# Performance work log

Hardware: AMD Instinct MI355X
Metric: run time of the kernel (lower is better)

## Reference

```python
import jax, jax.numpy as jnp
import numpy as np

NUM_HEADS = 12   # top-k = num_heads experts selected per token
SWITCHLOSS = 0.1
ZLOSS = 0.001


def setup_inputs() -> dict:
    key = jax.random.key(0)
    ks = jax.random.split(key, 8)
    B, N, C, E, D = 2, 2048, 768, 24, 64
    w = lambda k, shape: (jax.random.normal(k, shape, jnp.float32) * 0.02)
    return {
        "x": jax.random.normal(ks[0], (B, N, C), jnp.float32),
        "w_gate": w(ks[1], (C, E)),
        "W_in": w(ks[2], (E, C, D)),    # per-expert q projection
        "b_in": jnp.zeros((E, D), jnp.float32),
        "W_out": w(ks[3], (E, D, C)),   # per-expert output projection
        "b_out": jnp.zeros((E, C), jnp.float32),
        "W_kv": w(ks[4], (C, 2 * D)),   # shared single-head K/V
        "b_kv": jnp.zeros((2 * D,), jnp.float32),
    }


def reference(x, w_gate, W_in, b_in, W_out, b_out, W_kv, b_kv):
    B, N, C = x.shape
    E, _, D = W_in.shape
    H = NUM_HEADS
    scale = D ** -0.5

    xf = x.reshape(-1, C)                         # [T, C], T = B*N
    # --- top-k gating (k = num_heads) ---
    logits = xf @ w_gate                          # [T, E]
    probs = jax.nn.softmax(logits, axis=-1)
    top_p, idx = jax.lax.top_k(probs, H)          # [T, H]
    gates = top_p / (top_p.sum(-1, keepdims=True) + 1e-6)
    oh = jax.nn.one_hot(idx, E, dtype=x.dtype)    # [T, H, E]
    comb = oh * gates[..., None]                  # gated dispatch/combine weights

    # --- aux losses (switchloss + zloss; cvloss coeff = 0) ---
    dense_gates = comb.sum(1)                     # [T, E]
    freqs = (dense_gates > 0).astype(x.dtype).sum(0)
    p_sum = probs.sum(0)
    switch = E * jnp.sum((p_sum / p_sum.sum()) * (freqs / freqs.sum()))
    z = jnp.mean(jax.nn.logsumexp(logits, axis=1) ** 2)
    aux_loss = SWITCHLOSS * switch + ZLOSS * z

    # --- MoE map: per-token q via selected experts (no gate multiply) ---
    q_all = jnp.einsum('tc,ecd->ted', xf, W_in) + b_in     # [T, E, D]
    q = jnp.take_along_axis(q_all, idx[..., None], axis=1)  # [T, H, D]
    q = q.reshape(B, N, H, D)

    # --- shared-KV attention (multi-query style) ---
    kv = x @ W_kv + b_kv
    k, v = jnp.split(kv, 2, axis=-1)              # [B, N, D] each
    attn = jnp.einsum('bihd,bjd->bhij', q, k) * scale
    attn = jax.nn.softmax(attn, axis=-1)
    o = jnp.einsum('bhij,bjd->bihd', attn, v).reshape(-1, H, D)  # [T, H, D]

    # --- MoE reduce: gated combine through per-expert output projections ---
    xe = jnp.einsum('the,thd->ted', comb, o)      # [T, E, D] gated dispatch
    out = jnp.einsum('ted,edc->tc', xe, W_out) + jnp.einsum('the,ec->tc', comb, b_out)
    return out.reshape(B, N, C), aux_loss
```

## Files before the change

kernel.cpp:

```cpp
#include <hip/hip_runtime.h>
#include <hip/hip_bf16.h>

#define T_  4096
#define Bb  2
#define Nn  2048
#define Cc  768
#define Ee  24
#define Dd  64
#define Hh  12
#define KR  1600
#define KS  16
#define KC  48
#define NB2 1024
#define SCL 0.18033688f

typedef __attribute__((ext_vector_type(8))) short bf16x8;
typedef __attribute__((ext_vector_type(4))) short bf16x4;
typedef __attribute__((ext_vector_type(4))) float f32x4;
typedef __attribute__((ext_vector_type(8))) unsigned short u16x8;

__device__ __forceinline__ unsigned short f2bf(float f) {
  union { float f; unsigned int i; } u; u.f = f;
  unsigned int r = u.i + 0x7FFFu + ((u.i >> 16) & 1u);
  return (unsigned short)(r >> 16);
}

__device__ __forceinline__ void gload16(const void* g, void* l) {
  __builtin_amdgcn_global_load_lds(
      (const __attribute__((address_space(1))) void*)g,
      (__attribute__((address_space(3))) void*)l, 16, 0, 0);
}

#define XPAD 52
__global__ __launch_bounds__(256) void prep_kernel(
    const float* __restrict__ W_in, const float* __restrict__ W_out,
    const float* __restrict__ b_out, const float* __restrict__ W_kv,
    unsigned short* __restrict__ BqT, unsigned short* __restrict__ BrT,
    unsigned short* __restrict__ BkvT,
    const float* __restrict__ x, const float* __restrict__ wg,
    float* __restrict__ partial, unsigned short* __restrict__ xb)
{
  __shared__ __align__(16) float smem[64 * 129];
  const int bid = blockIdx.x, tid = threadIdx.x;

  if (bid < 900) {
    float* ls = smem;
    if (bid < 288) {
      const int e = bid / 12, c0 = (bid % 12) * 64;
      #pragma unroll
      for (int i = 0; i < 16; ++i) {
        int L = tid + i * 256, c = L >> 6, d = L & 63;
        ls[c * 65 + d] = W_in[(size_t)e * Cc * Dd + (size_t)(c0 + c) * Dd + d];
      }
      __syncthreads();
      #pragma unroll
      for (int i = 0; i < 16; ++i) {
        int L = tid + i * 256, d = L >> 6, c = L & 63;
        BqT[(size_t)(e * Dd + d) * Cc + c0 + c] = f2bf(ls[c * 65 + d]);
      }
    } else if (bid < 888) {
      const int i2 = bid - 288;
      const int k0 = (i2 / 12) * 32, n0 = (i2 % 12) * 64;
      #pragma unroll
      for (int i = 0; i < 8; ++i) {
        int L = tid + i * 256, k = L >> 6, n = L & 63;
        int kk = k0 + k;
        float v = (kk < 1536) ? W_out[(size_t)kk * Cc + n0 + n]
                : (kk < 1560) ? b_out[(size_t)(kk - 1536) * Cc + n0 + n] : 0.f;
        ls[k * 65 + n] = v;
      }
      __syncthreads();
      #pragma unroll
      for (int i = 0; i < 8; ++i) {
        int L = tid + i * 256, n = L >> 5, k = L & 31;
        BrT[(size_t)(n0 + n) * KR + k0 + k] = f2bf(ls[k * 65 + n]);
      }
    } else {
      const int c0 = (bid - 888) * 64;
      #pragma unroll
      for (int i = 0; i < 32; ++i) {
        int L = tid + i * 256, c = L >> 7, j = L & 127;
        ls[c * 129 + j] = W_kv[(size_t)(c0 + c) * 128 + j];
      }
      __syncthreads();
      #pragma unroll
      for (int i = 0; i < 32; ++i) {
        int L = tid + i * 256, j = L >> 6, c = L & 63;
        BkvT[(size_t)j * Cc + c0 + c] = f2bf(ls[c * 129 + j]);
      }
    }
  } else {
    float* xs  = smem;
    float* wsT = smem + 128 * XPAD;
    const int g = bid - 900;
    const int t0 = (g & 31) * 128;
    const int s = g >> 5, k0 = s * KC;

    #pragma unroll
    for (int i = 0; i < 6; ++i) {
      int f = tid + i * 256;
      int token = f / 12, j = f % 12;
      size_t gofs = (size_t)(t0 + token) * Cc + k0 + j * 4;
      float4 v = *(const float4*)&x[gofs];
      *(float4*)&xs[token * XPAD + j * 4] = v;
      ushort4 o;
      o.x = f2bf(v.x); o.y = f2bf(v.y); o.z = f2bf(v.z); o.w = f2bf(v.w);
      *(ushort4*)&xb[gofs] = o;
    }
    for (int i = tid; i < Ee * KC; i += 256)
      wsT[(i % Ee) * KC + i / Ee] = wg[k0 * Ee + i];
    __syncthreads();

    const int token = tid >> 1, half = tid & 1;
    float xr[KC];
    #pragma unroll
    for (int kg = 0; kg < KC / 4; ++kg)
      *(float4*)&xr[kg * 4] = *(const float4*)&xs[token * XPAD + kg * 4];

    float acc[12];
    #pragma unroll
    for (int e = 0; e < 12; ++e) acc[e] = 0.f;
    #pragma unroll
    for (int e = 0; e < 12; ++e) {
      const int eg = half * 12 + e;
      #pragma unroll
      for (int kg = 0; kg < KC / 4; ++kg) {
        float4 wv = *(const float4*)&wsT[eg * KC + kg * 4];
        acc[e] += xr[kg * 4 + 0] * wv.x + xr[kg * 4 + 1] * wv.y
                + xr[kg * 4 + 2] * wv.z + xr[kg * 4 + 3] * wv.w;
      }
    }

    float* dst = partial + ((size_t)(t0 + token) * KS + s) * Ee + half * 12;
    #pragma unroll
    for (int eg2 = 0; eg2 < 3; ++eg2)
      *(float4*)&dst[eg2 * 4] = *(float4*)&acc[eg2 * 4];
  }
}

template<int MODE>
__global__ __launch_bounds__(256) void gemm_bt_kernel(
    const unsigned short* __restrict__ A, const unsigned short* __restrict__ BT,
    const float* __restrict__ bias, const float* __restrict__ bias2,
    void* __restrict__ Cout, void* __restrict__ Cout2, void* __restrict__ Cout3,
    int K, int ldc)
{
  constexpr int BM = 64, BN = 64, MI = 2, NI = 2;
  __shared__ __align__(16) unsigned short As[2][BM * 64];
  __shared__ __align__(16) unsigned short Bs[2][BN * 64];
  const int tid = threadIdx.x, w = tid >> 6, lane = tid & 63;
  const int quad = lane >> 4, nl = lane & 15;
  const int m0 = blockIdx.x * BM, n0 = blockIdx.y * BN;
  const int mw = (w & 1) * 32, nw = (w >> 1) * 32;

  f32x4 acc[MI][NI];
  #pragma unroll
  for (int i = 0; i < MI; ++i)
    #pragma unroll
    for (int j = 0; j < NI; ++j) acc[i][j] = (f32x4){0.f, 0.f, 0.f, 0.f};

  const int sr  = lane >> 3;
  const int cbd = (lane & 7) ^ sr;
  const int xl  = nl & 7;
  const int ca0 = (quad ^ xl) * 8;
  const int ca1 = ((quad + 4) ^ xl) * 8;

  const unsigned short* abase = A + (size_t)(m0 + w * 16 + sr) * K + cbd * 8;
  const unsigned short* bbase = BT + (size_t)(n0 + w * 16 + sr) * K + cbd * 8;

  auto STAGE = [&](int bi, int k0) {
    #pragma unroll
    for (int i = 0; i < 2; ++i) {
      gload16(abase + (size_t)(i * 8) * K + k0, &As[bi][(w * 16 + i * 8) * 64]);
      gload16(bbase + (size_t)(i * 8) * K + k0, &Bs[bi][(w * 16 + i * 8) * 64]);
    }
  };

  const int nt = K / 64;
  STAGE(0, 0);
  __syncthreads();
  for (int t = 0; t < nt; ++t) {
    const int cur = t & 1;
    if (t + 1 < nt) STAGE(cur ^ 1, (t + 1) * 64);

    bf16x8 af0[MI], af1[MI], bf0[NI], bf1[NI];
    #pragma unroll
    for (int mi = 0; mi < MI; ++mi) {
      const unsigned short* ar = &As[cur][(mw + mi * 16 + nl) * 64];
      af0[mi] = *(const bf16x8*)(ar + ca0);
      af1[mi] = *(const bf16x8*)(ar + ca1);
    }
    #pragma unroll
    for (int ni = 0; ni < NI; ++ni) {
      const unsigned short* br = &Bs[cur][(nw + ni * 16 + nl) * 64];
      bf0[ni] = *(const bf16x8*)(br + ca0);
      bf1[ni] = *(const bf16x8*)(br + ca1);
    }
    #pragma unroll
    for (int mi = 0; mi < MI; ++mi)
      #pragma unroll
      for (int ni = 0; ni < NI; ++ni) {
        acc[mi][ni] = __builtin_amdgcn_mfma_f32_16x16x32_bf16(
            af0[mi], bf0[ni], acc[mi][ni], 0, 0, 0);
        acc[mi][ni] = __builtin_amdgcn_mfma_f32_16x16x32_bf16(
            af1[mi], bf1[ni], acc[mi][ni], 0, 0, 0);
      }

    __syncthreads();
  }

  #pragma unroll
  for (int mi = 0; mi < MI; ++mi) {
    int rowb = m0 + mw + mi * 16 + quad * 4;
    int bb = rowb >> 11, nn = rowb & (Nn - 1);
    #pragma unroll
    for (int ni = 0; ni < NI; ++ni) {
      int col = n0 + nw + ni * 16 + nl;
      if (MODE == 0) {
        #pragma unroll
        for (int reg = 0; reg < 4; ++reg)
          ((float*)Cout)[(size_t)(rowb + reg) * ldc + col] = acc[mi][ni][reg];
      } else {
        if (col < 1536) {
          float bv = bias[col];
          #pragma unroll
          for (int reg = 0; reg < 4; ++reg)
            ((unsigned short*)Cout)[(size_t)(rowb + reg) * 1536 + col] =
                f2bf((acc[mi][ni][reg] + bv) * SCL);
        } else {
          int c2 = col - 1536;
          float bv = bias2[c2];
          if (c2 < Dd) {
            #pragma unroll
            for (int reg = 0; reg < 4; ++reg)
              ((unsigned short*)Cout2)[((size_t)bb * Nn + nn + reg) * Dd + c2] =
                  f2bf(acc[mi][ni][reg] + bv);
          } else {
            int p6 = nn & 63;
            int np = (nn & ~63) | (p6 & 0x23)
                   | (((p6 >> 4) & 1) << 2) | (((p6 >> 2) & 3) << 3);
            ushort4 v;
            v.x = f2bf(acc[mi][ni][0] + bv);
            v.y = f2bf(acc[mi][ni][1] + bv);
            v.z = f2bf(acc[mi][ni][2] + bv);
            v.w = f2bf(acc[mi][ni][3] + bv);
            *(ushort4*)((unsigned short*)Cout3 +
                        ((size_t)bb * Dd + (c2 - Dd)) * Nn + np) = v;
          }
        }
      }
    }
  }
}

__global__ __launch_bounds__(256) void gate2_kernel(
    const float* __restrict__ partial,
    int* __restrict__ idx, float* __restrict__ gate, float* __restrict__ bstats,
    unsigned short* __restrict__ xeg)
{
  __shared__ float xls[4][KS * Ee];
  __shared__ float sacc[49];
  __shared__ unsigned short dens[4][64];
  const int tid = threadIdx.x;
  const int w = tid >> 6, lane = tid & 63;
  const int t = blockIdx.x * 4 + w;

  if (tid < 49) sacc[tid] = 0.f;
  dens[w][lane] = 0;

  const float* p = partial + (size_t)t * (KS * Ee);
  #pragma unroll
  for (int i = 0; i < 6; ++i) xls[w][lane + i * 64] = p[lane + i * 64];

  {
    u16x8 z = (u16x8){0, 0, 0, 0, 0, 0, 0, 0};
    unsigned short* xrow = xeg + (size_t)t * KR;
    #pragma unroll
    for (int i = 0; i < 3; ++i)
      *(u16x8*)&xrow[(lane + i * 64) * 8] = z;
  }

  float logit = -1e30f;
  if (lane < Ee) {
    float acc = 0.f;
    #pragma unroll
    for (int s = 0; s < KS; ++s) acc += xls[w][s * Ee + lane];
    logit = acc;
  }
  float m = logit;
  for (int o = 32; o; o >>= 1) m = fmaxf(m, __shfl_xor(m, o));
  float pr = (lane < Ee) ? expf(logit - m) : 0.f;
  float s = pr;
  for (int o = 32; o; o >>= 1) s += __shfl_xor(s, o);
  float prob = pr / s;
  float lse = m + logf(s);

  bool sel = false;
  float my_p = 0.f; int my_e = -1;
  for (int h = 0; h < Hh; ++h) {
    float v = (lane < Ee && !sel) ? prob : -1.f;
    int ix = lane;
    for (int o = 32; o; o >>= 1) {
      float ov = __shfl_xor(v, o); int oi = __shfl_xor(ix, o);
      if (ov > v || (ov == v && oi < ix)) { v = ov; ix = oi; }
    }
    if (lane == ix) sel = true;
    if (lane == h) { my_p = v; my_e = ix; }
  }
  float gsum = (lane < Hh) ? my_p : 0.f;
  for (int o = 32; o; o >>= 1) gsum += __shfl_xor(gsum, o);
  float gval = my_p / (gsum + 1e-6f);
  if (lane < Hh) {
    idx[t * Hh + lane] = my_e;
    gate[t * Hh + lane] = gval;
  }

  __syncthreads();
  if (lane < Ee) atomicAdd(&sacc[lane], prob);
  if (lane < Hh) {
    atomicAdd(&sacc[24 + my_e], 1.0f);
    dens[w][my_e] = f2bf(gval);
  }
  if (lane == 0) atomicAdd(&sacc[48], lse * lse);
  __syncthreads();
  if (tid < 49) bstats[(size_t)tid * NB2 + blockIdx.x] = sacc[tid];

  xeg[(size_t)t * KR + 1536 + lane] = dens[w][lane];
}

__global__ __launch_bounds__(256, 3) void attn_kernel(
    const unsigned short* __restrict__ qallb, const int* __restrict__ idx,
    const float* __restrict__ gate,
    const unsigned short* __restrict__ kbuf, const unsigned short* __restrict__ vtbuf,
    unsigned short* __restrict__ xeg)
{
  __shared__ __align__(16) unsigned short ksl[3][64 * 64];
  __shared__ __align__(16) unsigned short vtl[3][64 * 64];

  const int tid = threadIdx.x;
  const int w = tid >> 6, lane = tid & 63;
  const int quad = lane >> 4, nl = lane & 15;
  const int bh = blockIdx.y;
  const int b = bh / Hh, h = bh - b * Hh;
  const int qw = blockIdx.x * 64 + w * 16;

  const int tq = b * Nn + qw + nl;
  const int eq = idx[tq * Hh + h];
  const unsigned short* qrow = qallb + (size_t)tq * (Ee * Dd) + eq * Dd + quad * 8;
  const bf16x8 qB0 = *(const bf16x8*)(qrow);
  const bf16x8 qB1 = *(const bf16x8*)(qrow + 32);

  f32x4 acc[4];
  #pragma unroll
  for (int dg = 0; dg < 4; ++dg) acc[dg] = (f32x4){0.f, 0.f, 0.f, 0.f};
  float l = 0.f;

  const int sr  = lane >> 3;
  const int cbd = (lane & 7) ^ sr;
  const int xl  = nl & 7;
  const int ca0 = (quad ^ xl) * 8;
  const int ca1 = ((quad + 4) ^ xl) * 8;

  const unsigned short* kgbase =
      kbuf + ((size_t)b * Nn + w * 16 + sr) * Dd + cbd * 8;
  const unsigned short* vgbase =
      vtbuf + ((size_t)b * Dd + w * 16 + sr) * Nn + cbd * 8;

  auto STAGE = [&](int bi, int t) {
    const int j0 = t * 64;
    #pragma unroll
    for (int i = 0; i < 2; ++i) {
      gload16(kgbase + (size_t)(j0 + i * 8) * Dd, &ksl[bi][(w * 16 + i * 8) * 64]);
      gload16(vgbase + (size_t)(i * 8) * Nn + j0, &vtl[bi][(w * 16 + i * 8) * 64]);
    }
  };

  auto COMPUTE = [&](const unsigned short* ks_, const unsigned short* vt_) {
    __builtin_amdgcn_s_setprio(1);
    bf16x4 pf[4];
    #pragma unroll
    for (int kg = 0; kg < 4; ++kg) {
      const unsigned short* kr = ks_ + (kg * 16 + nl) * 64;
      bf16x8 a0 = *(const bf16x8*)(kr + ca0);
      bf16x8 a1 = *(const bf16x8*)(kr + ca1);
      f32x4 c = {0.f, 0.f, 0.f, 0.f};
      c = __builtin_amdgcn_mfma_f32_16x16x32_bf16(a0, qB0, c, 0, 0, 0);
      c = __builtin_amdgcn_mfma_f32_16x16x32_bf16(a1, qB1, c, 0, 0, 0);
      float p0 = __builtin_amdgcn_exp2f(c[0]);
      float p1 = __builtin_amdgcn_exp2f(c[1]);
      float p2 = __builtin_amdgcn_exp2f(c[2]);
      float p3 = __builtin_amdgcn_exp2f(c[3]);
      l += (p0 + p1) + (p2 + p3);
      union { __hip_bfloat162 h2[2]; bf16x4 v; } pk;
      pk.h2[0] = __float22bfloat162_rn(float2{p0, p1});
      pk.h2[1] = __float22bfloat162_rn(float2{p2, p3});
      pf[kg] = pk.v;
    }
    bf16x8 pb0 = __builtin_shufflevector(pf[0], pf[1], 0, 1, 2, 3, 4, 5, 6, 7);
    bf16x8 pb1 = __builtin_shufflevector(pf[2], pf[3], 0, 1, 2, 3, 4, 5, 6, 7);
    #pragma unroll
    for (int dg = 0; dg < 4; ++dg) {
      const unsigned short* vrow = vt_ + (dg * 16 + nl) * 64;
      bf16x8 v0 = *(const bf16x8*)(vrow + ca0);
      bf16x8 v1 = *(const bf16x8*)(vrow + ca1);
      acc[dg] = __builtin_amdgcn_mfma_f32_16x16x32_bf16(v0, pb0, acc[dg], 0, 0, 0);
      acc[dg] = __builtin_amdgcn_mfma_f32_16x16x32_bf16(v1, pb1, acc[dg], 0, 0, 0);
    }
    __builtin_amdgcn_s_setprio(0);
  };

  STAGE(0, 0);
  STAGE(1, 1);
  #pragma unroll 1
  for (int t = 0; t < 30; t += 3) {
    STAGE(2, t + 2);
    asm volatile("s_waitcnt vmcnt(8)" ::: "memory");
    __builtin_amdgcn_s_barrier();
    __builtin_amdgcn_sched_barrier(0);
    COMPUTE(ksl[0], vtl[0]);
    __builtin_amdgcn_sched_barrier(0);
    asm volatile("" ::: "memory");
    __builtin_amdgcn_s_barrier();

    STAGE(0, t + 3);
    asm volatile("s_waitcnt vmcnt(8)" ::: "memory");
    __builtin_amdgcn_s_barrier();
    __builtin_amdgcn_sched_barrier(0);
    COMPUTE(ksl[1], vtl[1]);
    __builtin_amdgcn_sched_barrier(0);
    asm volatile("" ::: "memory");
    __builtin_amdgcn_s_barrier();

    STAGE(1, t + 4);
    asm volatile("s_waitcnt vmcnt(8)" ::: "memory");
    __builtin_amdgcn_s_barrier();
    __builtin_amdgcn_sched_barrier(0);
    COMPUTE(ksl[2], vtl[2]);
    __builtin_amdgcn_sched_barrier(0);
    asm volatile("" ::: "memory");
    __builtin_amdgcn_s_barrier();
  }
  asm volatile("s_waitcnt vmcnt(4)" ::: "memory");
  __builtin_amdgcn_s_barrier();
  __builtin_amdgcn_sched_barrier(0);
  COMPUTE(ksl[0], vtl[0]);
  __builtin_amdgcn_sched_barrier(0);
  asm volatile("s_waitcnt vmcnt(0)" ::: "memory");
  __builtin_amdgcn_s_barrier();
  __builtin_amdgcn_sched_barrier(0);
  COMPUTE(ksl[1], vtl[1]);

  float lg = l;
  lg += __shfl_xor(lg, 16);
  lg += __shfl_xor(lg, 32);
  const float scale = gate[tq * Hh + h] / lg;
  unsigned short* xrow = xeg + (size_t)tq * KR + eq * Dd + quad * 4;
  #pragma unroll
  for (int dg = 0; dg < 4; ++dg) {
    ushort4 v;
    v.x = f2bf(acc[dg][0] * scale);
    v.y = f2bf(acc[dg][1] * scale);
    v.z = f2bf(acc[dg][2] * scale);
    v.w = f2bf(acc[dg][3] * scale);
    *(ushort4*)(xrow + dg * 16) = v;
  }
}

__global__ __launch_bounds__(256) void aux1_kernel(
    const float* __restrict__ bstats, float* __restrict__ stats2)
{
  __shared__ float r[4];
  const int j = blockIdx.x, tid = threadIdx.x;
  float4 v = *(const float4*)&bstats[(size_t)j * NB2 + tid * 4];
  float s = (v.x + v.y) + (v.z + v.w);
  for (int o = 32; o; o >>= 1) s += __shfl_xor(s, o);
  if ((tid & 63) == 0) r[tid >> 6] = s;
  __syncthreads();
  if (tid == 0) stats2[j] = (r[0] + r[1]) + (r[2] + r[3]);
}

__global__ void aux2_kernel(const float* __restrict__ stats2,
                            float* __restrict__ out, int out_size)
{
  const int lane = threadIdx.x;
  float a = (lane < Ee) ? stats2[lane] : 0.f;
  float b = (lane < Ee) ? stats2[24 + lane] : 0.f;
  float pt = a, ft = b, sw = a * b;
  for (int o = 32; o; o >>= 1) {
    pt += __shfl_xor(pt, o); ft += __shfl_xor(ft, o); sw += __shfl_xor(sw, o);
  }
  if (lane == 0) {
    float sswitch = (float)Ee * sw / (pt * ft);
    float z = stats2[48] * (1.0f / (float)T_);
    out[out_size - 1] = 0.1f * sswitch + 0.001f * z;
  }
}

extern "C" void kernel_launch(void* const* d_in, const int* in_sizes, int n_in,
                              void* d_out, int out_size, void* d_ws, size_t ws_size,
                              hipStream_t stream)
{
  const float* x     = (const float*)d_in[0];
  const float* wg    = (const float*)d_in[1];
  const float* W_in  = (const float*)d_in[2];
  const float* b_in  = (const float*)d_in[3];
  const float* W_out = (const float*)d_in[4];
  const float* b_out = (const float*)d_in[5];
  const float* W_kv  = (const float*)d_in[6];
  const float* b_kv  = (const float*)d_in[7];
  float* out = (float*)d_out;

  char* ws = (char*)d_ws;
  size_t off = 0;
  auto carve = [&](size_t bytes) -> void* {
    void* p = ws + off;
    off = (off + bytes + 255) & ~(size_t)255;
    return p;
  };
  int*            idx    = (int*)           carve((size_t)T_ * Hh * 4);
  float*          gate   = (float*)         carve((size_t)T_ * Hh * 4);
  float*          bstats = (float*)         carve((size_t)49 * NB2 * 4);
  float*          stats2 = (float*)         carve(256);
  float*          lgate  = (float*)         carve((size_t)T_ * KS * Ee * 4);
  unsigned short* xb     = (unsigned short*)carve((size_t)T_ * Cc * 2);
  unsigned short* BqkvT  = (unsigned short*)carve((size_t)(Ee * Dd + 128) * Cc * 2);
  unsigned short* BkvT   = BqkvT + (size_t)Ee * Dd * Cc;
  unsigned short* BrT    = (unsigned short*)carve((size_t)Cc * KR * 2);
  unsigned short* kbuf   = (unsigned short*)carve((size_t)T_ * Dd * 2);
  unsigned short* vtbuf  = (unsigned short*)carve((size_t)T_ * Dd * 2);
  unsigned short* qallb  = (unsigned short*)carve((size_t)T_ * Ee * Dd * 2);
  unsigned short* xeg    = (unsigned short*)carve((size_t)T_ * KR * 2);

  prep_kernel<<<1412, 256, 0, stream>>>(
      W_in, W_out, b_out, W_kv, BqkvT, BrT, BkvT, x, wg, lgate, xb);

  gate2_kernel<<<NB2, 256, 0, stream>>>(lgate, idx, gate, bstats, xeg);

  gemm_bt_kernel<1><<<dim3(T_ / 64, 26), 256, 0, stream>>>(
      xb, BqkvT, b_in, b_kv, qallb, kbuf, vtbuf, Cc, 1536);

  attn_kernel<<<dim3(Nn / 64, Bb * Hh), 256, 0, stream>>>(
      qallb, idx, gate, kbuf, vtbuf, xeg);

  gemm_bt_kernel<0><<<dim3(T_ / 64, Cc / 64), 256, 0, stream>>>(
      xeg, BrT, nullptr, nullptr, out, nullptr, nullptr, KR, Cc);

  aux1_kernel<<<49, 256, 0, stream>>>(bstats, stats2);
  aux2_kernel<<<1, 64, 0, stream>>>(stats2, out, out_size);
}
```

Measured before the change: 179.6 us.

## Merge independent gating and GEMM launches into combined heterogeneous grids

The gate-selection kernel and the QKV projection GEMM are folded into one launch, with blocks dispatching on block index, and the output GEMM is likewise merged with the first aux reduction. This removes two kernel launches and the gaps between them, letting independent work overlap on the device. The cost is that each merged kernel reserves the larger shared-memory footprint (32KB) for every block, including the lightweight gate and reduction blocks, which can lower occupancy for them.

```diff
diff --git a/kernel.cpp b/kernel.cpp
--- a/kernel.cpp
+++ b/kernel.cpp
@@ -139,18 +139,16 @@
 }
 
 template<int MODE>
-__global__ __launch_bounds__(256) void gemm_bt_kernel(
+__device__ __forceinline__ void gemm64_body(
+    int m0, int n0, unsigned short* AsB, unsigned short* BsB,
     const unsigned short* __restrict__ A, const unsigned short* __restrict__ BT,
     const float* __restrict__ bias, const float* __restrict__ bias2,
     void* __restrict__ Cout, void* __restrict__ Cout2, void* __restrict__ Cout3,
     int K, int ldc)
 {
-  constexpr int BM = 64, BN = 64, MI = 2, NI = 2;
-  __shared__ __align__(16) unsigned short As[2][BM * 64];
-  __shared__ __align__(16) unsigned short Bs[2][BN * 64];
+  constexpr int MI = 2, NI = 2;
   const int tid = threadIdx.x, w = tid >> 6, lane = tid & 63;
   const int quad = lane >> 4, nl = lane & 15;
-  const int m0 = blockIdx.x * BM, n0 = blockIdx.y * BN;
   const int mw = (w & 1) * 32, nw = (w >> 1) * 32;
 
   f32x4 acc[MI][NI];
@@ -171,8 +169,8 @@
   auto STAGE = [&](int bi, int k0) {
     #pragma unroll
     for (int i = 0; i < 2; ++i) {
-      gload16(abase + (size_t)(i * 8) * K + k0, &As[bi][(w * 16 + i * 8) * 64]);
-      gload16(bbase + (size_t)(i * 8) * K + k0, &Bs[bi][(w * 16 + i * 8) * 64]);
+      gload16(abase + (size_t)(i * 8) * K + k0, AsB + bi * 4096 + (w * 16 + i * 8) * 64);
+      gload16(bbase + (size_t)(i * 8) * K + k0, BsB + bi * 4096 + (w * 16 + i * 8) * 64);
     }
   };
 
@@ -183,16 +181,18 @@
     const int cur = t & 1;
     if (t + 1 < nt) STAGE(cur ^ 1, (t + 1) * 64);
 
+    const unsigned short* Ac = AsB + cur * 4096;
+    const unsigned short* Bc = BsB + cur * 4096;
     bf16x8 af0[MI], af1[MI], bf0[NI], bf1[NI];
     #pragma unroll
     for (int mi = 0; mi < MI; ++mi) {
-      const unsigned short* ar = &As[cur][(mw + mi * 16 + nl) * 64];
+      const unsigned short* ar = &Ac[(mw + mi * 16 + nl) * 64];
       af0[mi] = *(const bf16x8*)(ar + ca0);
       af1[mi] = *(const bf16x8*)(ar + ca1);
     }
     #pragma unroll
     for (int ni = 0; ni < NI; ++ni) {
-      const unsigned short* br = &Bs[cur][(nw + ni * 16 + nl) * 64];
+      const unsigned short* br = &Bc[(nw + ni * 16 + nl) * 64];
       bf0[ni] = *(const bf16x8*)(br + ca0);
       bf1[ni] = *(const bf16x8*)(br + ca1);
     }
@@ -253,24 +253,38 @@
   }
 }
 
-__global__ __launch_bounds__(256) void gate2_kernel(
-    const float* __restrict__ partial,
-    int* __restrict__ idx, float* __restrict__ gate, float* __restrict__ bstats,
+__global__ __launch_bounds__(256) void qkv_gate2_kernel(
+    const unsigned short* __restrict__ xb, const unsigned short* __restrict__ BqkvT,
+    const float* __restrict__ b_in, const float* __restrict__ b_kv,
+    unsigned short* __restrict__ qallb, unsigned short* __restrict__ kbuf,
+    unsigned short* __restrict__ vtbuf,
+    const float* __restrict__ partial, int* __restrict__ idx,
+    float* __restrict__ gate, float* __restrict__ bstats,
     unsigned short* __restrict__ xeg)
 {
-  __shared__ float xls[4][KS * Ee];
-  __shared__ float sacc[49];
-  __shared__ unsigned short dens[4][64];
-  const int tid = threadIdx.x;
+  __shared__ __align__(16) char smem[65536 / 2];
+  const int bid = blockIdx.x, tid = threadIdx.x;
+
+  if (bid >= NB2) {
+    const int b2 = bid - NB2;
+    const int m0 = (b2 & 63) * 64, n0 = (b2 >> 6) * 64;
+    gemm64_body<1>(m0, n0, (unsigned short*)smem, (unsigned short*)smem + 8192,
+                   xb, BqkvT, b_in, b_kv, qallb, kbuf, vtbuf, Cc, 1536);
+    return;
+  }
+
+  float* xls  = (float*)smem;
+  float* sacc = xls + 4 * KS * Ee;
+  unsigned short* dens = (unsigned short*)(sacc + 64);
   const int w = tid >> 6, lane = tid & 63;
-  const int t = blockIdx.x * 4 + w;
+  const int t = bid * 4 + w;
 
   if (tid < 49) sacc[tid] = 0.f;
-  dens[w][lane] = 0;
+  dens[w * 64 + lane] = 0;
 
   const float* p = partial + (size_t)t * (KS * Ee);
   #pragma unroll
-  for (int i = 0; i < 6; ++i) xls[w][lane + i * 64] = p[lane + i * 64];
+  for (int i = 0; i < 6; ++i) xls[w * (KS * Ee) + lane + i * 64] = p[lane + i * 64];
 
   {
     u16x8 z = (u16x8){0, 0, 0, 0, 0, 0, 0, 0};
@@ -284,7 +298,7 @@
   if (lane < Ee) {
     float acc = 0.f;
     #pragma unroll
-    for (int s = 0; s < KS; ++s) acc += xls[w][s * Ee + lane];
+    for (int s = 0; s < KS; ++s) acc += xls[w * (KS * Ee) + s * Ee + lane];
     logit = acc;
   }
   float m = logit;
@@ -319,13 +333,13 @@
   if (lane < Ee) atomicAdd(&sacc[lane], prob);
   if (lane < Hh) {
     atomicAdd(&sacc[24 + my_e], 1.0f);
-    dens[w][my_e] = f2bf(gval);
+    dens[w * 64 + my_e] = f2bf(gval);
   }
   if (lane == 0) atomicAdd(&sacc[48], lse * lse);
   __syncthreads();
-  if (tid < 49) bstats[(size_t)tid * NB2 + blockIdx.x] = sacc[tid];
-
-  xeg[(size_t)t * KR + 1536 + lane] = dens[w][lane];
+  if (tid < 49) bstats[(size_t)tid * NB2 + bid] = sacc[tid];
+
+  xeg[(size_t)t * KR + 1536 + lane] = dens[w * 64 + lane];
 }
 
 __global__ __launch_bounds__(256, 3) void attn_kernel(
@@ -466,17 +480,29 @@
   }
 }
 
-__global__ __launch_bounds__(256) void aux1_kernel(
+__global__ __launch_bounds__(256) void reduce_aux_kernel(
+    const unsigned short* __restrict__ xeg, const unsigned short* __restrict__ BrT,
+    float* __restrict__ out,
     const float* __restrict__ bstats, float* __restrict__ stats2)
 {
-  __shared__ float r[4];
-  const int j = blockIdx.x, tid = threadIdx.x;
-  float4 v = *(const float4*)&bstats[(size_t)j * NB2 + tid * 4];
-  float s = (v.x + v.y) + (v.z + v.w);
-  for (int o = 32; o; o >>= 1) s += __shfl_xor(s, o);
-  if ((tid & 63) == 0) r[tid >> 6] = s;
-  __syncthreads();
-  if (tid == 0) stats2[j] = (r[0] + r[1]) + (r[2] + r[3]);
+  __shared__ __align__(16) char smem[65536 / 2];
+  const int bid = blockIdx.x, tid = threadIdx.x;
+
+  if (bid >= 768) {
+    float* r = (float*)smem;
+    const int j = bid - 768;
+    float4 v = *(const float4*)&bstats[(size_t)j * NB2 + tid * 4];
+    float s = (v.x + v.y) + (v.z + v.w);
+    for (int o = 32; o; o >>= 1) s += __shfl_xor(s, o);
+    if ((tid & 63) == 0) r[tid >> 6] = s;
+    __syncthreads();
+    if (tid == 0) stats2[j] = (r[0] + r[1]) + (r[2] + r[3]);
+    return;
+  }
+
+  const int m0 = (bid & 63) * 64, n0 = (bid >> 6) * 64;
+  gemm64_body<0>(m0, n0, (unsigned short*)smem, (unsigned short*)smem + 8192,
+                 xeg, BrT, nullptr, nullptr, out, nullptr, nullptr, KR, Cc);
 }
 
 __global__ void aux2_kernel(const float* __restrict__ stats2,
@@ -534,17 +560,15 @@
   prep_kernel<<<1412, 256, 0, stream>>>(
       W_in, W_out, b_out, W_kv, BqkvT, BrT, BkvT, x, wg, lgate, xb);
 
-  gate2_kernel<<<NB2, 256, 0, stream>>>(lgate, idx, gate, bstats, xeg);
-
-  gemm_bt_kernel<1><<<dim3(T_ / 64, 26), 256, 0, stream>>>(
-      xb, BqkvT, b_in, b_kv, qallb, kbuf, vtbuf, Cc, 1536);
+  qkv_gate2_kernel<<<NB2 + (T_ / 64) * 26, 256, 0, stream>>>(
+      xb, BqkvT, b_in, b_kv, qallb, kbuf, vtbuf,
+      lgate, idx, gate, bstats, xeg);
 
   attn_kernel<<<dim3(Nn / 64, Bb * Hh), 256, 0, stream>>>(
       qallb, idx, gate, kbuf, vtbuf, xeg);
 
-  gemm_bt_kernel<0><<<dim3(T_ / 64, Cc / 64), 256, 0, stream>>>(
-      xeg, BrT, nullptr, nullptr, out, nullptr, nullptr, KR, Cc);
-
-  aux1_kernel<<<49, 256, 0, stream>>>(bstats, stats2);
+  reduce_aux_kernel<<<768 + 49, 256, 0, stream>>>(
+      xeg, BrT, out, bstats, stats2);
+
   aux2_kernel<<<1, 64, 0, stream>>>(stats2, out, out_size);
 }
```

Result: no change. 177.3 us (-1.3%).
